# Performance work log

Hardware: AMD Instinct MI355X
Metric: run time of the kernel (lower is better)

Reference implementation:

```python
import jax, jax.numpy as jnp
import numpy as np

B, S, D, H, F, E, K = 2, 2048, 1024, 16, 4096, 8, 2
EPS = 1e-6


def setup_inputs() -> dict:
    key = jax.random.key(0)
    ks = jax.random.split(key, 9)
    s = 0.02
    return {
        "x": jax.random.normal(ks[0], (B, S, D), jnp.float32),
        "n1_w": jnp.ones((D,), jnp.float32),
        "n2_w": jnp.ones((D,), jnp.float32),
        "wq": jax.random.normal(ks[1], (D, D), jnp.float32) * s,
        "wk": jax.random.normal(ks[2], (D, D), jnp.float32) * s,
        "wv": jax.random.normal(ks[3], (D, D), jnp.float32) * s,
        "wo": jax.random.normal(ks[4], (D, D), jnp.float32) * s,
        "router_w": jax.random.normal(ks[5], (E, D), jnp.float32) * s,  # nn.Linear(D, E, bias=False)
        "w1": jax.random.normal(ks[6], (E, D, F), jnp.float32) * s,
        "b1": jnp.zeros((E, F), jnp.float32),
        "w2": jax.random.normal(ks[7], (E, F, D), jnp.float32) * s,
        "b2": jnp.zeros((E, D), jnp.float32),
    }


def _rms(t, w):
    return t * w * jax.lax.rsqrt(jnp.mean(t * t, axis=-1, keepdims=True) + EPS)


def reference(x, n1_w, n2_w, wq, wk, wv, wo, router_w, w1, b1, w2, b2):
    hd = D // H
    # --- pre-norm causal multi-head self-attention ---
    h = _rms(x, n1_w)
    q = (h @ wq).reshape(B, S, H, hd)
    k = (h @ wk).reshape(B, S, H, hd)
    v = (h @ wv).reshape(B, S, H, hd)
    scores = jnp.einsum("bqhd,bkhd->bhqk", q, k) * (hd ** -0.5)
    causal = jnp.tril(jnp.ones((S, S), bool))
    scores = jnp.where(causal, scores, jnp.float32(-1e9))
    attn = jax.nn.softmax(scores, axis=-1)
    attn_out = jnp.einsum("bhqk,bkhd->bqhd", attn, v).reshape(B, S, D) @ wo
    x = x + attn_out
    # --- pre-norm MoE MLP: dense experts + top-k weighted combine ---
    h2 = _rms(x, n2_w)
    logits = h2 @ router_w.T                         # [B,S,E]
    probs = jax.nn.softmax(logits, axis=-1)
    topv, topi = jax.lax.top_k(probs, K)             # [B,S,K]
    topv = topv / jnp.sum(topv, axis=-1, keepdims=True)  # renormalized top-k gates
    bi = jnp.arange(B)[:, None, None]
    si = jnp.arange(S)[None, :, None]
    gates = jnp.zeros_like(probs).at[bi, si, topi].set(topv)  # sparse gates [B,S,E]
    eh = jax.nn.gelu(jnp.einsum("bsd,edf->ebsf", h2, w1) + b1[:, None, None, :])
    eo = jnp.einsum("ebsf,efd->ebsd", eh, w2) + b2[:, None, None, :]
    y = jnp.einsum("ebsd,bse->bsd", eo, gates)
    return x + y
```

## Files before the change

### kernel.cpp

```cpp
#include <hip/hip_runtime.h>
#include <hip/hip_bf16.h>


typedef float fx4 __attribute__((ext_vector_type(4)));
typedef short sx4 __attribute__((ext_vector_type(4)));
typedef short sx8 __attribute__((ext_vector_type(8)));
typedef int ix2 __attribute__((ext_vector_type(2)));
typedef int ix4 __attribute__((ext_vector_type(4)));

#define DEVFN static __device__ __forceinline__
#define MFMA16(a, b, c) __builtin_amdgcn_mfma_f32_16x16x32_bf16((a), (b), (c), 0, 0, 0)

typedef __attribute__((address_space(1))) const void GASV;
typedef __attribute__((address_space(3))) void LASV;

DEVFN short f2bf(float f) {
  unsigned u = __float_as_uint(f);
  return (short)((u + 0x7FFFu + ((u >> 16) & 1u)) >> 16);
}
DEVFN float bf2f(short s) { return __uint_as_float(((unsigned)(unsigned short)s) << 16); }

DEVFN int cvt_pk_bf16(float a, float b) {
  int r;
  asm("v_cvt_pk_bf16_f32 %0, %1, %2" : "=v"(r) : "v"(a), "v"(b));
  return r;
}

DEVFN void gll16(const short* g, short* l) {
  __builtin_amdgcn_global_load_lds((GASV*)g, (LASV*)l, 16, 0, 0);
}

DEVFN float fast_gelu(float x) {
  float u = 0.7978845608028654f * (x + 0.044715f * x * x * x);
  float e = __expf(2.0f * u);
  float t = 1.0f - 2.0f / (1.0f + e);
  return 0.5f * x * (1.0f + t);
}

DEVFN float wsum64(float v) {
#pragma unroll
  for (int m = 1; m < 64; m <<= 1) v += __shfl_xor(v, m);
  return v;
}

template <int SPLIT>
__global__ __launch_bounds__(256) void transpose_k(const float* in, short* oh, short* ol,
                                                   int R, int C) {
  __shared__ float t[64][65];
  const int c0 = blockIdx.x * 64, r0 = blockIdx.y * 64;
  const long long bofs = (long long)blockIdx.z * R * C;
  in += bofs;
  oh += bofs;
  if (SPLIT) ol += bofs;
  const int tid = threadIdx.x;
  const int rr = tid >> 4, cc4 = (tid & 15) * 4;
#pragma unroll
  for (int i = 0; i < 4; ++i) {
    int r = i * 16 + rr;
    fx4 v = *(const fx4*)(in + (long long)(r0 + r) * C + c0 + cc4);
    t[r][cc4] = v.x;
    t[r][cc4 + 1] = v.y;
    t[r][cc4 + 2] = v.z;
    t[r][cc4 + 3] = v.w;
  }
  __syncthreads();
#pragma unroll
  for (int i = 0; i < 4; ++i) {
    int oc = i * 16 + rr;
    sx4 hv, lv;
#pragma unroll
    for (int j = 0; j < 4; ++j) {
      float v = t[cc4 + j][oc];
      short hi = f2bf(v);
      hv[j] = hi;
      if (SPLIT) lv[j] = f2bf(v - bf2f(hi));
    }
    *(sx4*)(oh + (long long)(c0 + oc) * R + r0 + cc4) = hv;
    if (SPLIT) *(sx4*)(ol + (long long)(c0 + oc) * R + r0 + cc4) = lv;
  }
}

template <int SPLIT>
__global__ __launch_bounds__(256) void rms_k(const float* x, const float* w, short* hh,
                                             short* hl) {
  const int row = blockIdx.x, tid = threadIdx.x;
  const fx4 v = ((const fx4*)(x + (long long)row * 1024))[tid];
  float ss = v.x * v.x + v.y * v.y + v.z * v.z + v.w * v.w;
  ss = wsum64(ss);
  __shared__ float red[4];
  if ((tid & 63) == 0) red[tid >> 6] = ss;
  __syncthreads();
  ss = red[0] + red[1] + red[2] + red[3];
  const float rr = rsqrtf(ss * (1.0f / 1024.0f) + 1e-6f);
  const fx4 wv = ((const fx4*)w)[tid];
  float vals[4] = {v.x * wv.x * rr, v.y * wv.y * rr, v.z * wv.z * rr, v.w * wv.w * rr};
  sx4 oh, ol;
#pragma unroll
  for (int c = 0; c < 4; ++c) {
    short hi = f2bf(vals[c]);
    oh[c] = hi;
    if (SPLIT) ol[c] = f2bf(vals[c] - bf2f(hi));
  }
  ((sx4*)(hh + (long long)row * 1024))[tid] = oh;
  if (SPLIT) ((sx4*)(hl + (long long)row * 1024))[tid] = ol;
}

struct GemmArgs {
  const short *Ah, *Al, *Bh, *Bl;
  int K, lda, ldb, ldc;
  long long strideBe;
  short *out_h, *out_l;
  float* out_f;
  const float* resid;
  const float* bias;
  const int* tile_info;
  const int* n_tiles;
  const float* row_gate;
};

template <int TERMS, int BK, int EPI, int PIPE>
__global__ __launch_bounds__(256) void gemm_k(GemmArgs a) {
  const int tid = threadIdx.x, lane = tid & 63, wave = tid >> 6;
  const int gx = gridDim.x;
  const int nwg = gx * (int)gridDim.y;
  int flat = (int)blockIdx.y * gx + (int)blockIdx.x;
  flat = (flat & 7) * (nwg >> 3) + (flat >> 3);
  const int bx = flat % gx;
  const int by = flat / gx;

  int row0, expert = 0, valid = 128;
  if constexpr (EPI >= 3) {
    if (by >= *a.n_tiles) return;
    const int* ti = a.tile_info + by * 4;
    expert = ti[0];
    row0 = ti[1];
    valid = ti[2];
  } else {
    row0 = by * 128;
  }
  const short* Ap = a.Ah;
  const short* Bp = a.Bh + (EPI >= 3 ? (long long)expert * a.strideBe : 0ll);

  constexpr int CH = BK / 8;
  constexpr int SW = (BK == 64) ? 7 : 3;
  constexpr int NI = BK / 16;
  constexpr int TSZ = 128 * BK;
  constexpr int NB = PIPE ? 2 : 1;

  __shared__ short Ash[NB][TSZ];
  __shared__ short Bsh[NB][TSZ];
  __shared__ short Asl[TERMS == 3 ? NB : 1][TERMS == 3 ? TSZ : 1];
  __shared__ short Bsl[TERMS == 3 ? NB : 1][TERMS == 3 ? TSZ : 1];

  fx4 acc[4][4] = {};
  const int wr = wave >> 1, wc = wave & 1;

  auto stage = [&](int s, int k0) {
#pragma unroll
    for (int i = 0; i < NI; ++i) {
      int t = i * 256 + tid;
      int row = t / CH, c = t % CH;
      int cc = c ^ (row & SW);
      int lbase = (i * 256 + wave * 64) * 8;
      long long acol = k0 + cc * 8;
      gll16(Ap + (long long)(row0 + row) * a.lda + acol, &Ash[s][lbase]);
      gll16(Bp + (long long)(bx * 128 + row) * a.ldb + acol, &Bsh[s][lbase]);
      if constexpr (TERMS == 3) {
        gll16(a.Al + (long long)(row0 + row) * a.lda + acol, &Asl[s][lbase]);
        gll16(a.Bl + (long long)(bx * 128 + row) * a.ldb + acol, &Bsl[s][lbase]);
      }
    }
  };

  auto compute = [&](int s) {
#pragma unroll
    for (int kk = 0; kk < BK / 32; ++kk) {
      sx8 ah[4], bh[4], al_[4], bl_[4];
#pragma unroll
      for (int mi = 0; mi < 4; ++mi) {
        int row = wr * 64 + mi * 16 + (lane & 15);
        int sc = (kk * 4 + (lane >> 4)) ^ (row & SW);
        ah[mi] = *(const sx8*)&Ash[s][row * BK + sc * 8];
        if constexpr (TERMS == 3) al_[mi] = *(const sx8*)&Asl[s][row * BK + sc * 8];
      }
#pragma unroll
      for (int ni = 0; ni < 4; ++ni) {
        int row = wc * 64 + ni * 16 + (lane & 15);
        int sc = (kk * 4 + (lane >> 4)) ^ (row & SW);
        bh[ni] = *(const sx8*)&Bsh[s][row * BK + sc * 8];
        if constexpr (TERMS == 3) bl_[ni] = *(const sx8*)&Bsl[s][row * BK + sc * 8];
      }
#pragma unroll
      for (int mi = 0; mi < 4; ++mi)
#pragma unroll
        for (int ni = 0; ni < 4; ++ni) {
          acc[mi][ni] = MFMA16(ah[mi], bh[ni], acc[mi][ni]);
          if constexpr (TERMS == 3) {
            acc[mi][ni] = MFMA16(ah[mi], bl_[ni], acc[mi][ni]);
            acc[mi][ni] = MFMA16(al_[mi], bh[ni], acc[mi][ni]);
          }
        }
    }
  };

  const int NT = a.K / BK;
  stage(0, 0);
  __syncthreads();
  for (int t = 0; t < NT; ++t) {
    if constexpr (PIPE) {
      if (t + 1 < NT) stage((t + 1) & 1, (t + 1) * BK);
      compute(t & 1);
      if (t + 1 < NT) __syncthreads();
    } else {
      compute(0);
      if (t + 1 < NT) {
        __syncthreads();
        stage(0, (t + 1) * BK);
        __syncthreads();
      }
    }
  }

#pragma unroll
  for (int mi = 0; mi < 4; ++mi)
#pragma unroll
    for (int ni = 0; ni < 4; ++ni) {
      fx4 v = acc[mi][ni];
      int rl = wr * 64 + mi * 16 + ((lane >> 4) << 2);
      int col = bx * 128 + wc * 64 + ni * 16 + (lane & 15);
#pragma unroll
      for (int j = 0; j < 4; ++j) {
        int r = rl + j;
        long long grow = (long long)row0 + r;
        float xv = v[j];
        if constexpr (EPI == 1) {
          short hi = f2bf(xv);
          a.out_h[grow * a.ldc + col] = hi;
          a.out_l[grow * a.ldc + col] = f2bf(xv - bf2f(hi));
        } else if constexpr (EPI == 2) {
          a.out_f[grow * a.ldc + col] = xv + a.resid[grow * a.ldc + col];
        } else if constexpr (EPI == 3) {
          xv += a.bias[expert * a.ldc + col];
          a.out_h[grow * a.ldc + col] = f2bf(fast_gelu(xv));
        } else if constexpr (EPI == 5) {
          if (r < valid) {
            xv += a.bias[expert * a.ldc + col];
            float g = a.row_gate[grow];
            a.out_h[grow * a.ldc + col] = f2bf(xv * g);
          }
        }
      }
    }
}

__global__ __launch_bounds__(256) void combine_k(const int* row_of_entry,
                                                 const short* eo, float* out) {
  const int tid = threadIdx.x, lane = tid & 63, wave = tid >> 6;
  const long long token = (long long)blockIdx.x * 4 + wave;
  const int r1 = row_of_entry[token * 2];
  const int r2 = row_of_entry[token * 2 + 1];
  const sx8* e1 = (const sx8*)(eo + (long long)r1 * 1024);
  const sx8* e2 = (const sx8*)(eo + (long long)r2 * 1024);
  float* op = out + token * 1024;
#pragma unroll
  for (int half = 0; half < 2; ++half) {
    sx8 va = e1[lane + half * 64];
    sx8 vb = e2[lane + half * 64];
    int cb = (lane + half * 64) * 8;
#pragma unroll
    for (int q = 0; q < 2; ++q) {
      fx4 o = *(const fx4*)(op + cb + q * 4);
#pragma unroll
      for (int j = 0; j < 4; ++j) o[j] += bf2f(va[q * 4 + j]) + bf2f(vb[q * 4 + j]);
      *(fx4*)(op + cb + q * 4) = o;
    }
  }
}

__global__ __launch_bounds__(128, 2) void flash_k(const short* __restrict__ qkv_h,
                                                  const short* __restrict__ qkv_l,
                                                  short* __restrict__ ao_h,
                                                  short* __restrict__ ao_l) {
  const int tid = threadIdx.x, lane = tid & 63, wave = tid >> 6;
  const int l15 = lane & 15, g = lane >> 4;
  const int qt = (blockIdx.x + blockIdx.y) & 31;
  const int bh = blockIdx.y;
  const int b = bh >> 4, h = bh & 15;
  const long long base = (long long)b * 2048 * 3072;
  const int qw = qt * 64 + wave * 32;

  __shared__ short Kh[4096], Kl[4096];
  __shared__ int VTh[64 * 34], VTl[64 * 34];

  sx8 qh[2][2], ql[2][2];
#pragma unroll
  for (int mb = 0; mb < 2; ++mb)
#pragma unroll
    for (int kk = 0; kk < 2; ++kk) {
      long long qofs =
          base + (long long)(qw + mb * 16 + l15) * 3072 + h * 64 + kk * 32 + g * 8;
      qh[mb][kk] = *(const sx8*)(qkv_h + qofs);
      ql[mb][kk] = *(const sx8*)(qkv_l + qofs);
    }

  fx4 o[2][4] = {};
  float m_r[2] = {-3e38f, -3e38f}, l_r[2] = {0.f, 0.f};

  const int krow0 = tid >> 3;
  const int kc8 = (tid & 7) * 8;
  const int kswz = ((tid & 7) ^ (krow0 & 7)) * 8;
  const int vu = tid >> 3;
  const int vd0 = (tid & 7) * 8;

  sx8 kr[4], krl[4], vr[4], vrl[4];

  auto load_tile = [&](int kt2) {
    const long long tb = base + (long long)(kt2 * 64) * 3072 + h * 64;
#pragma unroll
    for (int s = 0; s < 4; ++s) {
      long long gofs = tb + 1024 + (long long)(s * 16 + krow0) * 3072 + kc8;
      kr[s] = *(const sx8*)(qkv_h + gofs);
      krl[s] = *(const sx8*)(qkv_l + gofs);
    }
#pragma unroll
    for (int k4 = 0; k4 < 4; ++k4) {
      long long gofs = tb + 2048 + (long long)(4 * vu + k4) * 3072 + vd0;
      vr[k4] = *(const sx8*)(qkv_h + gofs);
      vrl[k4] = *(const sx8*)(qkv_l + gofs);
    }
  };

  const int nt = qt + 1;
  load_tile(0);

  for (int kt = 0; kt < nt; ++kt) {
#pragma unroll
    for (int s = 0; s < 4; ++s) {
      *(sx8*)&Kh[(s * 16 + krow0) * 64 + kswz] = kr[s];
      *(sx8*)&Kl[(s * 16 + krow0) * 64 + kswz] = krl[s];
    }
#pragma unroll
    for (int i = 0; i < 8; ++i) {
      int d = vd0 + i;
      ix2 wh, wl;
      wh[0] = (int)(unsigned short)vr[0][i] | ((int)(unsigned short)vr[1][i] << 16);
      wh[1] = (int)(unsigned short)vr[2][i] | ((int)(unsigned short)vr[3][i] << 16);
      wl[0] = (int)(unsigned short)vrl[0][i] | ((int)(unsigned short)vrl[1][i] << 16);
      wl[1] = (int)(unsigned short)vrl[2][i] | ((int)(unsigned short)vrl[3][i] << 16);
      *(ix2*)&VTh[d * 34 + 2 * vu] = wh;
      *(ix2*)&VTl[d * 34 + 2 * vu] = wl;
    }
    __syncthreads();

    if (kt + 1 < nt) load_tile(kt + 1);

    const bool diag = (kt == nt - 1);
    float pvv[2][16];
#pragma unroll
    for (int kc = 0; kc < 4; ++kc) {
      int row = kc * 16 + l15;
      int rsw = row & 7;
      fx4 s0 = {}, s1 = {};
#pragma unroll
      for (int kk = 0; kk < 2; ++kk) {
        int sc = ((kk * 4 + g) ^ rsw) * 8;
        sx8 khf = *(const sx8*)&Kh[row * 64 + sc];
        sx8 klf = *(const sx8*)&Kl[row * 64 + sc];
        s0 = MFMA16(khf, qh[0][kk], s0);
        s1 = MFMA16(khf, qh[1][kk], s1);
        s0 = MFMA16(khf, ql[0][kk], s0);
        s1 = MFMA16(khf, ql[1][kk], s1);
        s0 = MFMA16(klf, qh[0][kk], s0);
        s1 = MFMA16(klf, qh[1][kk], s1);
      }
#pragma unroll
      for (int j = 0; j < 4; ++j) {
        pvv[0][kc * 4 + j] = s0[j];
        pvv[1][kc * 4 + j] = s1[j];
      }
    }

    sx8 pah[2][2], pal[2][2];
#pragma unroll
    for (int mb = 0; mb < 2; ++mb) {
      const int qidx = qw + mb * 16 + l15;
      float t[16];
      float tmax = -3e38f;
#pragma unroll
      for (int i = 0; i < 16; ++i) {
        float sv = pvv[mb][i] * 0.18033688011112f;
        if (diag) {
          int key = kt * 64 + (i >> 2) * 16 + g * 4 + (i & 3);
          sv = (key > qidx) ? -3e38f : sv;
        }
        t[i] = sv;
        tmax = fmaxf(tmax, sv);
      }
      tmax = fmaxf(tmax, __shfl_xor(tmax, 16));
      tmax = fmaxf(tmax, __shfl_xor(tmax, 32));
      if (__any(tmax > m_r[mb] + 8.0f)) {
        float mnew = fmaxf(m_r[mb], tmax);
        float al = exp2f(m_r[mb] - mnew);
        l_r[mb] *= al;
        float aj[4];
#pragma unroll
        for (int j = 0; j < 4; ++j) aj[j] = __shfl(al, (lane & 48) | (g << 2) | j);
#pragma unroll
        for (int f = 0; f < 4; ++f)
#pragma unroll
          for (int j = 0; j < 4; ++j) o[mb][f][j] *= aj[j];
        m_r[mb] = mnew;
      }
      float ps = 0.f;
#pragma unroll
      for (int i = 0; i < 16; ++i) {
        float e = exp2f(t[i] - m_r[mb]);
        t[i] = e;
        ps += e;
      }
      l_r[mb] += ps;
#pragma unroll
      for (int grp = 0; grp < 2; ++grp) {
        ix4 ih, il;
#pragma unroll
        for (int q2 = 0; q2 < 4; ++q2) {
          float a = t[grp * 8 + 2 * q2], bb = t[grp * 8 + 2 * q2 + 1];
          int I = cvt_pk_bf16(a, bb);
          float h0 = __uint_as_float((unsigned)I << 16);
          float h1 = __uint_as_float((unsigned)I & 0xffff0000u);
          int L = cvt_pk_bf16(a - h0, bb - h1);
          ih[q2] = I;
          il[q2] = L;
        }
        pah[mb][grp] = __builtin_bit_cast(sx8, ih);
        pal[mb][grp] = __builtin_bit_cast(sx8, il);
      }
    }

    const ix2* vth = (const ix2*)VTh;
    const ix2* vtl = (const ix2*)VTl;
#pragma unroll
    for (int f = 0; f < 4; ++f) {
      int dd = f * 16 + l15;
      ix2 a0 = vth[dd * 17 + g], a1 = vth[dd * 17 + 4 + g];
      ix2 a2 = vth[dd * 17 + 8 + g], a3 = vth[dd * 17 + 12 + g];
      ix2 c0 = vtl[dd * 17 + g], c1 = vtl[dd * 17 + 4 + g];
      ix2 c2 = vtl[dd * 17 + 8 + g], c3 = vtl[dd * 17 + 12 + g];
      ix4 w;
      w[0] = a0[0]; w[1] = a0[1]; w[2] = a1[0]; w[3] = a1[1];
      sx8 vh8a = __builtin_bit_cast(sx8, w);
      w[0] = a2[0]; w[1] = a2[1]; w[2] = a3[0]; w[3] = a3[1];
      sx8 vh8b = __builtin_bit_cast(sx8, w);
      w[0] = c0[0]; w[1] = c0[1]; w[2] = c1[0]; w[3] = c1[1];
      sx8 vl8a = __builtin_bit_cast(sx8, w);
      w[0] = c2[0]; w[1] = c2[1]; w[2] = c3[0]; w[3] = c3[1];
      sx8 vl8b = __builtin_bit_cast(sx8, w);
#pragma unroll
      for (int mb = 0; mb < 2; ++mb) {
        o[mb][f] = MFMA16(pah[mb][0], vh8a, o[mb][f]);
        o[mb][f] = MFMA16(pah[mb][0], vl8a, o[mb][f]);
        o[mb][f] = MFMA16(pal[mb][0], vh8a, o[mb][f]);
        o[mb][f] = MFMA16(pah[mb][1], vh8b, o[mb][f]);
        o[mb][f] = MFMA16(pah[mb][1], vl8b, o[mb][f]);
        o[mb][f] = MFMA16(pal[mb][1], vh8b, o[mb][f]);
      }
    }
    __syncthreads();
  }

#pragma unroll
  for (int mb = 0; mb < 2; ++mb) {
    float lt = l_r[mb];
    lt += __shfl_xor(lt, 16);
    lt += __shfl_xor(lt, 32);
    float linv = 1.0f / lt;
    float lj[4];
#pragma unroll
    for (int j = 0; j < 4; ++j) lj[j] = __shfl(linv, (lane & 48) | (g << 2) | j);
#pragma unroll
    for (int f = 0; f < 4; ++f)
#pragma unroll
      for (int j = 0; j < 4; ++j) {
        float val = o[mb][f][j] * lj[j];
        long long orow = (long long)b * 2048 + qw + mb * 16 + g * 4 + j;
        int ocol = h * 64 + f * 16 + l15;
        short hi = f2bf(val);
        ao_h[orow * 1024 + ocol] = hi;
        ao_l[orow * 1024 + ocol] = f2bf(val - bf2f(hi));
      }
  }
}

__global__ __launch_bounds__(256) void router_k(const float* x2, const float* w,
                                                const float* rw, int* tok_e,
                                                float* tok_g) {
  const int tid = threadIdx.x, lane = tid & 63, wave = tid >> 6;
  const long long token = (long long)blockIdx.x * 4 + wave;
  const fx4* xr = (const fx4*)(x2 + token * 1024);
  const fx4* wr4 = (const fx4*)w;
  fx4 t[4];
  float ss = 0.0f;
#pragma unroll
  for (int i = 0; i < 4; ++i) {
    fx4 xv = xr[i * 64 + lane];
    fx4 wv = wr4[i * 64 + lane];
    ss += xv.x * xv.x + xv.y * xv.y + xv.z * xv.z + xv.w * xv.w;
    t[i].x = xv.x * wv.x;
    t[i].y = xv.y * wv.y;
    t[i].z = xv.z * wv.z;
    t[i].w = xv.w * wv.w;
  }
  ss = wsum64(ss);
  const float rr = rsqrtf(ss * (1.0f / 1024.0f) + 1e-6f);
  float logit[8];
#pragma unroll
  for (int e = 0; e < 8; ++e) {
    const fx4* re = (const fx4*)(rw + e * 1024);
    float acc = 0.0f;
#pragma unroll
    for (int i = 0; i < 4; ++i) {
      fx4 rv = re[i * 64 + lane];
      acc += t[i].x * rv.x + t[i].y * rv.y + t[i].z * rv.z + t[i].w * rv.w;
    }
    logit[e] = wsum64(acc) * rr;
  }
  float mx = logit[0];
#pragma unroll
  for (int e = 1; e < 8; ++e) mx = fmaxf(mx, logit[e]);
  float pe[8];
#pragma unroll
  for (int e = 0; e < 8; ++e) pe[e] = expf(logit[e] - mx);
  int e1 = 0;
  float b1v = pe[0];
#pragma unroll
  for (int e = 1; e < 8; ++e)
    if (pe[e] > b1v) {
      b1v = pe[e];
      e1 = e;
    }
  int e2 = -1;
  float b2v = -1.0f;
#pragma unroll
  for (int e = 0; e < 8; ++e)
    if (e != e1 && pe[e] > b2v) {
      b2v = pe[e];
      e2 = e;
    }
  if (lane == 0) {
    float inv = 1.0f / (b1v + b2v);
    tok_e[token * 2] = e1;
    tok_e[token * 2 + 1] = e2;
    tok_g[token * 2] = b1v * inv;
    tok_g[token * 2 + 1] = b2v * inv;
  }
}

__global__ __launch_bounds__(1024) void rank_k(const int* tok_e, const float* tok_g,
                                               int* tinfo, int* ntv, int* row_of_entry,
                                               int* row_token, float* row_gate) {
  const int tid = threadIdx.x, lane = tid & 63, wave = tid >> 6;
  __shared__ unsigned wtot[16][4];
  __shared__ unsigned woff[16][4];
  __shared__ int segsh[8];
  int e[8];
  {
    const int4* te = (const int4*)tok_e;
    int4 a = te[tid * 2], b = te[tid * 2 + 1];
    e[0] = a.x; e[1] = a.y; e[2] = a.z; e[3] = a.w;
    e[4] = b.x; e[5] = b.y; e[6] = b.z; e[7] = b.w;
  }
  unsigned c0 = 0, c1 = 0, c2 = 0, c3 = 0;
#pragma unroll
  for (int i = 0; i < 8; ++i) {
    unsigned f = 1u << ((e[i] & 1) << 4);
    int h = e[i] >> 1;
    c0 += (h == 0) ? f : 0u;
    c1 += (h == 1) ? f : 0u;
    c2 += (h == 2) ? f : 0u;
    c3 += (h == 3) ? f : 0u;
  }
  unsigned s0 = c0, s1 = c1, s2 = c2, s3 = c3;
#pragma unroll
  for (int d = 1; d < 64; d <<= 1) {
    unsigned t0 = __shfl_up(s0, d), t1 = __shfl_up(s1, d);
    unsigned t2 = __shfl_up(s2, d), t3 = __shfl_up(s3, d);
    if (lane >= d) { s0 += t0; s1 += t1; s2 += t2; s3 += t3; }
  }
  if (lane == 63) {
    wtot[wave][0] = s0; wtot[wave][1] = s1; wtot[wave][2] = s2; wtot[wave][3] = s3;
  }
  __syncthreads();
  if (wave == 0 && lane < 16) {
    unsigned v0 = wtot[lane][0], v1 = wtot[lane][1];
    unsigned v2 = wtot[lane][2], v3 = wtot[lane][3];
    unsigned i0 = v0, i1 = v1, i2 = v2, i3 = v3;
#pragma unroll
    for (int d = 1; d < 16; d <<= 1) {
      unsigned t0 = __shfl_up(i0, d), t1 = __shfl_up(i1, d);
      unsigned t2 = __shfl_up(i2, d), t3 = __shfl_up(i3, d);
      if (lane >= d) { i0 += t0; i1 += t1; i2 += t2; i3 += t3; }
    }
    woff[lane][0] = i0 - v0; woff[lane][1] = i1 - v1;
    woff[lane][2] = i2 - v2; woff[lane][3] = i3 - v3;
    if (lane == 15) {
      wtot[0][0] = i0; wtot[0][1] = i1; wtot[0][2] = i2; wtot[0][3] = i3;
    }
  }
  __syncthreads();
  if (tid == 0) {
    int off = 0, nt = 0;
    for (int ee = 0; ee < 8; ++ee) {
      unsigned tot = wtot[0][ee >> 1];
      int c = (int)((tot >> ((ee & 1) * 16)) & 0xFFFFu);
      segsh[ee] = off;
      int tt = (c + 127) >> 7;
      for (int i = 0; i < tt; ++i) {
        tinfo[nt * 4 + 0] = ee;
        tinfo[nt * 4 + 1] = off + i * 128;
        int v = c - i * 128;
        tinfo[nt * 4 + 2] = v > 128 ? 128 : v;
        tinfo[nt * 4 + 3] = 0;
        ++nt;
      }
      off += tt << 7;
    }
    *ntv = nt;
  }
  __syncthreads();
  unsigned x0 = woff[wave][0] + s0 - c0;
  unsigned x1 = woff[wave][1] + s1 - c1;
  unsigned x2 = woff[wave][2] + s2 - c2;
  unsigned x3 = woff[wave][3] + s3 - c3;
  const int entry0 = tid * 8;
#pragma unroll
  for (int i = 0; i < 8; ++i) {
    int ee = e[i];
    int h = ee >> 1, sh = (ee & 1) << 4;
    unsigned px = (h == 0) ? x0 : (h == 1) ? x1 : (h == 2) ? x2 : x3;
    int rank = (int)((px >> sh) & 0xFFFFu);
    unsigned f = 1u << sh;
    x0 += (h == 0) ? f : 0u;
    x1 += (h == 1) ? f : 0u;
    x2 += (h == 2) ? f : 0u;
    x3 += (h == 3) ? f : 0u;
    int row = segsh[ee] + rank;
    row_of_entry[entry0 + i] = row;
    row_token[row] = (entry0 + i) >> 1;
    row_gate[row] = tok_g[entry0 + i];
  }
}

__global__ __launch_bounds__(256) void gather_copy_k(const int* row_of_entry,
                                                     const short* h2, short* h2g) {
  const int tid = threadIdx.x, lane = tid & 63, wave = tid >> 6;
  const int entry = blockIdx.x * 4 + wave;
  const int token = entry >> 1;
  const int r = row_of_entry[entry];
  const sx8* src = (const sx8*)(h2 + (long long)token * 1024);
  sx8* dst = (sx8*)(h2g + (long long)r * 1024);
  dst[lane] = src[lane];
  dst[lane + 64] = src[lane + 64];
}

extern "C" void kernel_launch(void* const* d_in, const int* in_sizes, int n_in,
                              void* d_out, int out_size, void* d_ws, size_t ws_size,
                              hipStream_t stream) {
  (void)in_sizes;
  (void)n_in;
  (void)out_size;
  (void)ws_size;
  const float* x = (const float*)d_in[0];
  const float* n1w = (const float*)d_in[1];
  const float* n2w = (const float*)d_in[2];
  const float* wq = (const float*)d_in[3];
  const float* wk = (const float*)d_in[4];
  const float* wv = (const float*)d_in[5];
  const float* wo = (const float*)d_in[6];
  const float* rw = (const float*)d_in[7];
  const float* w1 = (const float*)d_in[8];
  const float* b1 = (const float*)d_in[9];
  const float* w2 = (const float*)d_in[10];
  const float* b2 = (const float*)d_in[11];
  float* out = (float*)d_out;
  char* ws = (char*)d_ws;

  short* wqkv_h = (short*)(ws + 0);
  short* wqkv_l = (short*)(ws + 6291456);
  short* wo_h = (short*)(ws + 12582912);
  short* wo_l = (short*)(ws + 14680064);
  short* h_h = (short*)(ws + 16777216);
  short* h_l = (short*)(ws + 25165824);
  short* qkv_h = (short*)(ws + 33554432);
  short* qkv_l = (short*)(ws + 58720256);
  short* ao_h = (short*)(ws + 83886080);
  short* ao_l = (short*)(ws + 92274688);
  short* h2 = (short*)(ws + 0);
  short* h2g = (short*)(ws + 8388608);
  short* eo = (short*)(ws + 8388608);
  short* wslot = (short*)(ws + 27262976);
  int* row_of_entry = (int*)(ws + 94371840);
  short* eh = (short*)(ws + 100663296);
  char* ctrl = ws + 176160768;
  int* ntv = (int*)(ctrl + 96);
  int* tinfo = (int*)(ctrl + 128);
  int* tok_e = (int*)(ctrl + 2048);
  float* tok_g = (float*)(ctrl + 2048 + 32768);
  int* row_token = (int*)(ctrl + 2048 + 65536);
  float* row_gate = (float*)(ctrl + 2048 + 65536 + 36864);

  transpose_k<1><<<dim3(16, 16, 1), 256, 0, stream>>>(wq, wqkv_h, wqkv_l, 1024, 1024);
  transpose_k<1><<<dim3(16, 16, 1), 256, 0, stream>>>(wk, wqkv_h + 1024 * 1024,
                                                      wqkv_l + 1024 * 1024, 1024, 1024);
  transpose_k<1><<<dim3(16, 16, 1), 256, 0, stream>>>(wv, wqkv_h + 2048 * 1024,
                                                      wqkv_l + 2048 * 1024, 1024, 1024);
  transpose_k<1><<<dim3(16, 16, 1), 256, 0, stream>>>(wo, wo_h, wo_l, 1024, 1024);

  rms_k<1><<<4096, 256, 0, stream>>>(x, n1w, h_h, h_l);

  {
    GemmArgs a = {};
    a.Ah = h_h;
    a.Al = h_l;
    a.Bh = wqkv_h;
    a.Bl = wqkv_l;
    a.K = 1024;
    a.lda = 1024;
    a.ldb = 1024;
    a.ldc = 3072;
    a.out_h = qkv_h;
    a.out_l = qkv_l;
    gemm_k<3, 32, 1, 1><<<dim3(24, 32), 256, 0, stream>>>(a);
  }

  flash_k<<<dim3(32, 32), 128, 0, stream>>>(qkv_h, qkv_l, ao_h, ao_l);

  {
    GemmArgs a = {};
    a.Ah = ao_h;
    a.Al = ao_l;
    a.Bh = wo_h;
    a.Bl = wo_l;
    a.K = 1024;
    a.lda = 1024;
    a.ldb = 1024;
    a.ldc = 1024;
    a.out_f = out;
    a.resid = x;
    gemm_k<3, 32, 2, 1><<<dim3(8, 32), 256, 0, stream>>>(a);
  }

  rms_k<0><<<4096, 256, 0, stream>>>(out, n2w, h2, nullptr);
  router_k<<<1024, 256, 0, stream>>>(out, n2w, rw, tok_e, tok_g);
  rank_k<<<1, 1024, 0, stream>>>(tok_e, tok_g, tinfo, ntv, row_of_entry, row_token,
                                 row_gate);
  gather_copy_k<<<2048, 256, 0, stream>>>(row_of_entry, h2, h2g);

  transpose_k<0><<<dim3(64, 16, 8), 256, 0, stream>>>(w1, wslot, nullptr, 1024, 4096);
  {
    GemmArgs a = {};
    a.Ah = h2g;
    a.Bh = wslot;
    a.K = 1024;
    a.lda = 1024;
    a.ldb = 1024;
    a.ldc = 4096;
    a.strideBe = (long long)4096 * 1024;
    a.out_h = eh;
    a.bias = b1;
    a.tile_info = tinfo;
    a.n_tiles = ntv;
    gemm_k<1, 64, 3, 0><<<dim3(32, 80), 256, 0, stream>>>(a);
  }

  transpose_k<0><<<dim3(16, 64, 8), 256, 0, stream>>>(w2, wslot, nullptr, 4096, 1024);
  {
    GemmArgs a = {};
    a.Ah = eh;
    a.Bh = wslot;
    a.K = 4096;
    a.lda = 4096;
    a.ldb = 4096;
    a.ldc = 1024;
    a.strideBe = (long long)1024 * 4096;
    a.out_h = eo;
    a.bias = b2;
    a.tile_info = tinfo;
    a.n_tiles = ntv;
    a.row_gate = row_gate;
    gemm_k<1, 64, 5, 0><<<dim3(8, 80), 256, 0, stream>>>(a);
  }

  combine_k<<<1024, 256, 0, stream>>>(row_of_entry, eo, out);
}
```

Measured before the change: 752.0 us.

## Split-K the output projection, spread expert tiles evenly, pipeline second expert GEMM

The wo projection GEMM is split along K into two halves over blockIdx.z, writing fp32 partials that a new elementwise kernel sums with the residual. This doubles the workgroup count for a GEMM that otherwise launches only 256 tiles. The router ranking now spreads the active expert tiles across all 80 grid slots and marks empty slots with valid=0, replacing the early exit on a tile counter. The second expert GEMM also switches to the double-buffered pipelined variant, which uses more LDS. The price is extra partial-sum memory traffic and one more kernel launch.

```diff
diff --git a/kernel.cpp b/kernel.cpp
--- a/kernel.cpp
+++ b/kernel.cpp
@@ -111,10 +111,8 @@
   long long strideBe;
   short *out_h, *out_l;
   float* out_f;
-  const float* resid;
   const float* bias;
   const int* tile_info;
-  const int* n_tiles;
   const float* row_gate;
 };
 
@@ -129,17 +127,18 @@
   const int by = flat / gx;
 
   int row0, expert = 0, valid = 128;
-  if constexpr (EPI >= 3) {
-    if (by >= *a.n_tiles) return;
+  if constexpr (EPI == 3 || EPI == 5) {
     const int* ti = a.tile_info + by * 4;
     expert = ti[0];
     row0 = ti[1];
     valid = ti[2];
+    if (valid == 0) return;
   } else {
     row0 = by * 128;
   }
   const short* Ap = a.Ah;
-  const short* Bp = a.Bh + (EPI >= 3 ? (long long)expert * a.strideBe : 0ll);
+  const short* Bp = a.Bh + ((EPI == 3 || EPI == 5) ? (long long)expert * a.strideBe : 0ll);
+  const int kbeg = blockIdx.z * a.K;
 
   constexpr int CH = BK / 8;
   constexpr int SW = (BK == 64) ? 7 : 3;
@@ -162,7 +161,7 @@
       int row = t / CH, c = t % CH;
       int cc = c ^ (row & SW);
       int lbase = (i * 256 + wave * 64) * 8;
-      long long acol = k0 + cc * 8;
+      long long acol = kbeg + k0 + cc * 8;
       gll16(Ap + (long long)(row0 + row) * a.lda + acol, &Ash[s][lbase]);
       gll16(Bp + (long long)(bx * 128 + row) * a.ldb + acol, &Bsh[s][lbase]);
       if constexpr (TERMS == 3) {
@@ -237,8 +236,6 @@
           short hi = f2bf(xv);
           a.out_h[grow * a.ldc + col] = hi;
           a.out_l[grow * a.ldc + col] = f2bf(xv - bf2f(hi));
-        } else if constexpr (EPI == 2) {
-          a.out_f[grow * a.ldc + col] = xv + a.resid[grow * a.ldc + col];
         } else if constexpr (EPI == 3) {
           xv += a.bias[expert * a.ldc + col];
           a.out_h[grow * a.ldc + col] = f2bf(fast_gelu(xv));
@@ -248,9 +245,23 @@
             float g = a.row_gate[grow];
             a.out_h[grow * a.ldc + col] = f2bf(xv * g);
           }
+        } else if constexpr (EPI == 6) {
+          a.out_f[(long long)blockIdx.z * 4194304 + grow * a.ldc + col] = xv;
         }
       }
     }
+}
+
+__global__ __launch_bounds__(256) void combine_wo_k(const float* p0, const float* p1,
+                                                    const float* resid, float* out) {
+  const long long i = ((long long)blockIdx.x * 256 + threadIdx.x) * 4;
+  fx4 a = *(const fx4*)(p0 + i);
+  fx4 b = *(const fx4*)(p1 + i);
+  fx4 r = *(const fx4*)(resid + i);
+  fx4 o;
+#pragma unroll
+  for (int j = 0; j < 4; ++j) o[j] = a[j] + b[j] + r[j];
+  *(fx4*)(out + i) = o;
 }
 
 __global__ __launch_bounds__(256) void combine_k(const int* row_of_entry,
@@ -556,7 +567,7 @@
 }
 
 __global__ __launch_bounds__(1024) void rank_k(const int* tok_e, const float* tok_g,
-                                               int* tinfo, int* ntv, int* row_of_entry,
+                                               int* tinfo, int* row_of_entry,
                                                int* row_token, float* row_gate) {
   const int tid = threadIdx.x, lane = tid & 63, wave = tid >> 6;
   __shared__ unsigned wtot[16][4];
@@ -608,23 +619,27 @@
   }
   __syncthreads();
   if (tid == 0) {
-    int off = 0, nt = 0;
+    int cnt[8], tte[8], total = 0;
     for (int ee = 0; ee < 8; ++ee) {
       unsigned tot = wtot[0][ee >> 1];
-      int c = (int)((tot >> ((ee & 1) * 16)) & 0xFFFFu);
+      cnt[ee] = (int)((tot >> ((ee & 1) * 16)) & 0xFFFFu);
+      tte[ee] = (cnt[ee] + 127) >> 7;
+      total += tte[ee];
+    }
+    for (int s2 = 0; s2 < 80; ++s2) tinfo[s2 * 4 + 2] = 0;
+    int off = 0, i = 0;
+    for (int ee = 0; ee < 8; ++ee) {
       segsh[ee] = off;
-      int tt = (c + 127) >> 7;
-      for (int i = 0; i < tt; ++i) {
-        tinfo[nt * 4 + 0] = ee;
-        tinfo[nt * 4 + 1] = off + i * 128;
-        int v = c - i * 128;
-        tinfo[nt * 4 + 2] = v > 128 ? 128 : v;
-        tinfo[nt * 4 + 3] = 0;
-        ++nt;
-      }
-      off += tt << 7;
-    }
-    *ntv = nt;
+      for (int t2 = 0; t2 < tte[ee]; ++t2) {
+        int slot = (i * 80) / total;
+        tinfo[slot * 4 + 0] = ee;
+        tinfo[slot * 4 + 1] = off + t2 * 128;
+        int v = cnt[ee] - t2 * 128;
+        tinfo[slot * 4 + 2] = v > 128 ? 128 : v;
+        ++i;
+      }
+      off += tte[ee] << 7;
+    }
   }
   __syncthreads();
   unsigned x0 = woff[wave][0] + s0 - c0;
@@ -694,6 +709,7 @@
   short* qkv_l = (short*)(ws + 58720256);
   short* ao_h = (short*)(ws + 83886080);
   short* ao_l = (short*)(ws + 92274688);
+  float* wo_part = (float*)(ws + 100663296);
   short* h2 = (short*)(ws + 0);
   short* h2g = (short*)(ws + 8388608);
   short* eo = (short*)(ws + 8388608);
@@ -701,7 +717,6 @@
   int* row_of_entry = (int*)(ws + 94371840);
   short* eh = (short*)(ws + 100663296);
   char* ctrl = ws + 176160768;
-  int* ntv = (int*)(ctrl + 96);
   int* tinfo = (int*)(ctrl + 128);
   int* tok_e = (int*)(ctrl + 2048);
   float* tok_g = (float*)(ctrl + 2048 + 32768);
@@ -740,18 +755,18 @@
     a.Al = ao_l;
     a.Bh = wo_h;
     a.Bl = wo_l;
-    a.K = 1024;
+    a.K = 512;
     a.lda = 1024;
     a.ldb = 1024;
     a.ldc = 1024;
-    a.out_f = out;
-    a.resid = x;
-    gemm_k<3, 32, 2, 1><<<dim3(8, 32), 256, 0, stream>>>(a);
-  }
+    a.out_f = wo_part;
+    gemm_k<3, 32, 6, 1><<<dim3(8, 32, 2), 256, 0, stream>>>(a);
+  }
+  combine_wo_k<<<4096, 256, 0, stream>>>(wo_part, wo_part + 4194304, x, out);
 
   rms_k<0><<<4096, 256, 0, stream>>>(out, n2w, h2, nullptr);
   router_k<<<1024, 256, 0, stream>>>(out, n2w, rw, tok_e, tok_g);
-  rank_k<<<1, 1024, 0, stream>>>(tok_e, tok_g, tinfo, ntv, row_of_entry, row_token,
+  rank_k<<<1, 1024, 0, stream>>>(tok_e, tok_g, tinfo, row_of_entry, row_token,
                                  row_gate);
   gather_copy_k<<<2048, 256, 0, stream>>>(row_of_entry, h2, h2g);
 
@@ -768,7 +783,6 @@
     a.out_h = eh;
     a.bias = b1;
     a.tile_info = tinfo;
-    a.n_tiles = ntv;
     gemm_k<1, 64, 3, 0><<<dim3(32, 80), 256, 0, stream>>>(a);
   }
 
@@ -785,9 +799,8 @@
     a.out_h = eo;
     a.bias = b2;
     a.tile_info = tinfo;
-    a.n_tiles = ntv;
     a.row_gate = row_gate;
-    gemm_k<1, 64, 5, 0><<<dim3(8, 80), 256, 0, stream>>>(a);
+    gemm_k<1, 64, 5, 1><<<dim3(8, 80), 256, 0, stream>>>(a);
   }
 
   combine_k<<<1024, 256, 0, stream>>>(row_of_entry, eo, out);
```

Result: faster. 706.1 us (-6.1%).
